# Kernel tuning notes

Hardware: AMD Instinct MI355X
Metric: run time of the kernel (lower is better)

The kernel has to match this reference:

```python
import jax, jax.numpy as jnp
import numpy as np

N, IN_C, E = 50000, 512, 800000
H, C = 2, 64          # heads, per-head channels
HC = H * C            # 128
OUT_C = 2
B = 64                # number of graphs
EPS = 1e-5
NEG_SLOPE = 0.2


def gat_conv(x, src, dst, W, a_src, a_dst, bias):
    """PyG GATConv (concat=True, add_self_loops already included in src/dst)."""
    n = x.shape[0]
    h = (x @ W).reshape(n, H, C)                      # [N,H,C]
    alpha_src = (h * a_src[None]).sum(-1)             # [N,H]
    alpha_dst = (h * a_dst[None]).sum(-1)             # [N,H]
    e = jax.nn.leaky_relu(alpha_src[src] + alpha_dst[dst], NEG_SLOPE)  # [E,H]
    # segment softmax over incoming edges of each destination node
    m = jax.ops.segment_max(e, dst, num_segments=n)   # [N,H]
    ex = jnp.exp(e - m[dst])
    denom = jax.ops.segment_sum(ex, dst, num_segments=n)
    alpha = ex / denom[dst]                           # [E,H]
    msg = h[src] * alpha[:, :, None]                  # [E,H,C]
    out = jax.ops.segment_sum(msg, dst, num_segments=n)  # [N,H,C]
    return out.reshape(n, HC) + bias


def batch_norm(x, gamma, beta):
    # BatchNorm1d in training mode: batch statistics over the node dim
    mu = x.mean(0)
    var = x.var(0)
    return gamma * (x - mu) * jax.lax.rsqrt(var + EPS) + beta


def setup_inputs() -> dict:
    key = jax.random.key(0)
    ks = jax.random.split(key, 16)
    x = jax.random.normal(ks[0], (N, IN_C), dtype=jnp.float32)
    edge_index = jax.random.randint(ks[1], (2, E), 0, N, dtype=jnp.int64)
    batch = jnp.sort(jax.random.randint(ks[2], (N,), 0, B, dtype=jnp.int64))
    g = lambda k, sh, fan: jax.random.normal(k, sh, dtype=jnp.float32) * (1.0 / np.sqrt(fan))
    return {
        "x": x, "edge_index": edge_index, "batch": batch,
        "W1": g(ks[3], (IN_C, HC), IN_C),
        "att_src1": g(ks[4], (H, C), C), "att_dst1": g(ks[5], (H, C), C),
        "b1": jnp.zeros((HC,), jnp.float32),
        "gamma1": jnp.ones((HC,), jnp.float32), "beta1": jnp.zeros((HC,), jnp.float32),
        "W2": g(ks[6], (HC, HC), HC),
        "att_src2": g(ks[7], (H, C), C), "att_dst2": g(ks[8], (H, C), C),
        "b2": jnp.zeros((HC,), jnp.float32),
        "gamma2": jnp.ones((HC,), jnp.float32), "beta2": jnp.zeros((HC,), jnp.float32),
        "Wlin": g(ks[9], (HC, OUT_C), HC),
        "blin": jnp.zeros((OUT_C,), jnp.float32),
    }


def reference(x, edge_index, batch, W1, att_src1, att_dst1, b1, gamma1, beta1,
              W2, att_src2, att_dst2, b2, gamma2, beta2, Wlin, blin):
    n = x.shape[0]
    # GATConv adds self-loops by default
    loop = jnp.arange(n, dtype=edge_index.dtype)
    src = jnp.concatenate([edge_index[0], loop])
    dst = jnp.concatenate([edge_index[1], loop])

    h = gat_conv(x, src, dst, W1, att_src1, att_dst1, b1)
    h = jax.nn.relu(batch_norm(h, gamma1, beta1))
    h = gat_conv(h, src, dst, W2, att_src2, att_dst2, b2)
    h = jax.nn.relu(batch_norm(h, gamma2, beta2))

    # global mean pool over graphs
    sums = jax.ops.segment_sum(h, batch, num_segments=B)           # [B,HC]
    cnt = jax.ops.segment_sum(jnp.ones((n,), h.dtype), batch, num_segments=B)
    pooled = sums / jnp.maximum(cnt, 1.0)[:, None]
    return pooled @ Wlin + blin                                    # [B,OUT_C]
```

## Files before the change

kernel.cpp:

```cpp
#include <hip/hip_runtime.h>
#include <hip/hip_bf16.h>
#include <cstdint>
#include <cstddef>

#define NN      50000
#define IN_C    512
#define EE      800000
#define ETOT    850000
#define HH      2
#define CC      64
#define HC      128
#define BB      64
#define OUTC    2
#define NEG_SLOPE 0.2f
#define BN_EPS  1e-5f

#define NBLK_SCAN ((NN + 255) / 256)

#define NXCD     8
#define NPX      ((NN + NXCD - 1) / NXCD)
#define EDGES_PER_SLOT 2048
#define NSLOT    ((ETOT + EDGES_PER_SLOT - 1) / EDGES_PER_SLOT)
#define WFRG_BLKS ((IN_C * 16 + HC * 16 + 255) / 256)

typedef __bf16 bf16x8 __attribute__((ext_vector_type(8)));
typedef float  f32x4  __attribute__((ext_vector_type(4)));

__device__ __forceinline__ unsigned f2bf(float f) {
    __bf16 b = (__bf16)f;
    return (unsigned)__builtin_bit_cast(unsigned short, b);
}

__device__ __forceinline__ void gload_lds16(const float* g, float* l) {
    __builtin_amdgcn_global_load_lds(
        (const __attribute__((address_space(1))) unsigned*)g,
        (__attribute__((address_space(3))) unsigned*)l,
        16, 0, 0);
}

__global__ __launch_bounds__(256) void prep_kernel(
    const float* __restrict__ W1, unsigned short* __restrict__ Wf1,
    const float* __restrict__ W2, unsigned short* __restrict__ Wf2,
    const int* __restrict__ ei, int* __restrict__ deg)
{
    if (blockIdx.x < WFRG_BLKS) {
        int t = blockIdx.x * 256 + threadIdx.x;
        const float* W; unsigned short* Wf;
        if (t < IN_C * 16) { W = W1; Wf = Wf1; }
        else {
            t -= IN_C * 16;
            if (t >= HC * 16) return;
            W = W2; Wf = Wf2;
        }
        int lane = t & 63, frag = t >> 6;
        int kblk = frag >> 3, nt = frag & 7;
        int quad = lane >> 4, ln = lane & 15;
        int kbase = kblk * 32 + quad * 8;
        int n = nt * 16 + ln;
        unsigned short u[8];
#pragma unroll
        for (int j = 0; j < 8; ++j)
            u[j] = (unsigned short)f2bf(W[(size_t)(kbase + j) * HC + n]);
        ushort4 a; a.x = u[0]; a.y = u[1]; a.z = u[2]; a.w = u[3];
        ushort4 b; b.x = u[4]; b.y = u[5]; b.z = u[6]; b.w = u[7];
        *(ushort4*)(Wf + (size_t)t * 8)     = a;
        *(ushort4*)(Wf + (size_t)t * 8 + 4) = b;
        return;
    }
    const int bid  = blockIdx.x - WFRG_BLKS;
    const int xcd  = bid & (NXCD - 1);
    const int slot = bid >> 3;
    const int lo = xcd * NPX, hi = lo + NPX;
    const int base = slot * EDGES_PER_SLOT;
#pragma unroll
    for (int it = 0; it < EDGES_PER_SLOT / 256; ++it) {
        int e = base + it * 256 + threadIdx.x;
        if (e < ETOT) {
            int d = (e < EE) ? ei[EE + e] : (e - EE);
            if (d >= lo && d < hi) atomicAdd(&deg[d], 1);
        }
    }
}

__global__ __launch_bounds__(256) void bsum_kernel(const int* __restrict__ deg, int* __restrict__ bsum)
{
    int i = blockIdx.x * 256 + threadIdx.x;
    int v = (i < NN) ? deg[i] : 0;
    int lane = threadIdx.x & 63, wv = threadIdx.x >> 6;
#pragma unroll
    for (int o = 32; o > 0; o >>= 1) v += __shfl_down(v, o);
    __shared__ int ws[4];
    if (lane == 0) ws[wv] = v;
    __syncthreads();
    if (threadIdx.x == 0) bsum[blockIdx.x] = ws[0] + ws[1] + ws[2] + ws[3];
}

__global__ __launch_bounds__(256) void bscan_kernel(
    const int* __restrict__ bsum, int* __restrict__ bofs, int* __restrict__ rowp)
{
    int t = threadIdx.x;
    int lane = t & 63, wv = t >> 6;
    int v = (t < NBLK_SCAN) ? bsum[t] : 0;
    int x = v;
#pragma unroll
    for (int o = 1; o < 64; o <<= 1) {
        int y = __shfl_up(x, o);
        if (lane >= o) x += y;
    }
    __shared__ int ws[4];
    if (lane == 63) ws[wv] = x;
    __syncthreads();
    int wo = 0;
#pragma unroll
    for (int w = 0; w < 4; ++w) if (w < wv) wo += ws[w];
    if (t < NBLK_SCAN) bofs[t] = x + wo - v;
    if (t == 0) rowp[NN] = ETOT;
}

__global__ __launch_bounds__(256) void bapply_kernel(
    const int* __restrict__ deg, const int* __restrict__ bofs,
    int* __restrict__ rowp, int* __restrict__ cur)
{
    int i = blockIdx.x * 256 + threadIdx.x;
    int v = (i < NN) ? deg[i] : 0;
    int lane = threadIdx.x & 63, wv = threadIdx.x >> 6;
    int x = v;
#pragma unroll
    for (int o = 1; o < 64; o <<= 1) {
        int y = __shfl_up(x, o);
        if (lane >= o) x += y;
    }
    __shared__ int ws[4];
    if (lane == 63) ws[wv] = x;
    __syncthreads();
    int wo = 0;
#pragma unroll
    for (int w = 0; w < 4; ++w) if (w < wv) wo += ws[w];
    if (i < NN) {
        int r = bofs[blockIdx.x] + x + wo - v;
        rowp[i] = r; cur[i] = r;
    }
}

__global__ __launch_bounds__(256) void scatter_kernel(
    const int* __restrict__ ei, int* __restrict__ cur, int* __restrict__ esrc)
{
    const int xcd  = blockIdx.x & (NXCD - 1);
    const int slot = blockIdx.x >> 3;
    const int lo = xcd * NPX, hi = lo + NPX;
    const int base = slot * EDGES_PER_SLOT;
#pragma unroll
    for (int it = 0; it < EDGES_PER_SLOT / 256; ++it) {
        int e = base + it * 256 + threadIdx.x;
        if (e < ETOT) {
            int s, d;
            if (e < EE) { s = ei[e]; d = ei[EE + e]; }
            else        { s = e - EE; d = s; }
            if (d >= lo && d < hi) {
                int pos = atomicAdd(&cur[d], 1);
                esrc[pos] = s;
            }
        }
    }
}

template<int K, bool AFFINE>
__global__ __launch_bounds__(256) void mfma_gemm_kernel(
    const float* __restrict__ A, const unsigned short* __restrict__ Wf,
    const float* __restrict__ atts, const float* __restrict__ attd,
    unsigned* __restrict__ hb, float* __restrict__ as_, float* __restrict__ ad_,
    const float* __restrict__ sc, const float* __restrict__ sh)
{
    constexpr int NSTEP = K >> 5;
    __shared__ __align__(16) float Abuf[2][64 * 64];

    const int tid  = threadIdx.x;
    const int wave = tid >> 6, lane = tid & 63;
    const int quad = lane >> 4, ln = lane & 15;
    const int m0 = blockIdx.x * 64;

    const int srow = tid >> 3;
    const int g    = (tid & 7) ^ (srow & 7);
    int grow0 = m0 + srow;      if (grow0 > NN - 1) grow0 = NN - 1;
    int grow1 = m0 + srow + 32; if (grow1 > NN - 1) grow1 = NN - 1;
    const float* gsrc0 = A + (size_t)grow0 * K + g * 4;
    const float* gsrc1 = A + (size_t)grow1 * K + g * 4;

    const int rr = wave * 16 + ln;
    const int base_f = rr * 32;
    const int sA = (((quad * 2)     ^ (rr & 7)) * 4);
    const int sB = (((quad * 2 + 1) ^ (rr & 7)) * 4);

    const unsigned short* wbase = Wf + lane * 8;

    f32x4 acc[8];
#pragma unroll
    for (int nt = 0; nt < 8; ++nt) acc[nt] = (f32x4){0.f, 0.f, 0.f, 0.f};

    gload_lds16(gsrc0,      &Abuf[0][wave * 256]);
    gload_lds16(gsrc1,      &Abuf[0][1024 + wave * 256]);
    gload_lds16(gsrc0 + 32, &Abuf[0][2048 + wave * 256]);
    gload_lds16(gsrc1 + 32, &Abuf[0][3072 + wave * 256]);
    bf16x8 bfr[2][8];
#pragma unroll
    for (int nt = 0; nt < 8; ++nt) bfr[0][nt] = *(const bf16x8*)(wbase + nt * 512);

#pragma unroll
    for (int ks = 0; ks < NSTEP; ++ks) {
        const int sub  = ks & 1;
        const int cbuf = (ks >> 1) & 1;
        const int bsel = ks & 1;
        if (sub == 0) {
            __syncthreads();
            if (ks + 2 < NSTEP) {
                const float* n0 = gsrc0 + (size_t)(ks + 2) * 32;
                const float* n1 = gsrc1 + (size_t)(ks + 2) * 32;
                float* db = &Abuf[cbuf ^ 1][wave * 256];
                gload_lds16(n0,      db);
                gload_lds16(n1,      db + 1024);
                gload_lds16(n0 + 32, db + 2048);
                gload_lds16(n1 + 32, db + 3072);
            }
        }

        const float* fb_base = &Abuf[cbuf][sub * 2048 + base_f];
        float4 fa = *(const float4*)(fb_base + sA);
        float4 fb = *(const float4*)(fb_base + sB);
        float va[8] = {fa.x, fa.y, fa.z, fa.w, fb.x, fb.y, fb.z, fb.w};
        if (AFFINE) {
            const int kk = ks * 32 + quad * 8;
            const float4 s0 = *(const float4*)(sc + kk), s1 = *(const float4*)(sc + kk + 4);
            const float4 h0 = *(const float4*)(sh + kk), h1 = *(const float4*)(sh + kk + 4);
            va[0] = fmaxf(fmaf(s0.x, va[0], h0.x), 0.f);
            va[1] = fmaxf(fmaf(s0.y, va[1], h0.y), 0.f);
            va[2] = fmaxf(fmaf(s0.z, va[2], h0.z), 0.f);
            va[3] = fmaxf(fmaf(s0.w, va[3], h0.w), 0.f);
            va[4] = fmaxf(fmaf(s1.x, va[4], h1.x), 0.f);
            va[5] = fmaxf(fmaf(s1.y, va[5], h1.y), 0.f);
            va[6] = fmaxf(fmaf(s1.z, va[6], h1.z), 0.f);
            va[7] = fmaxf(fmaf(s1.w, va[7], h1.w), 0.f);
        }
        union { bf16x8 v; unsigned short u[8]; } af;
#pragma unroll
        for (int j = 0; j < 8; ++j) af.u[j] = (unsigned short)f2bf(va[j]);

        if (ks + 1 < NSTEP) {
            const unsigned short* wfp = wbase + (size_t)(ks + 1) * 4096;
#pragma unroll
            for (int nt = 0; nt < 8; ++nt)
                bfr[bsel ^ 1][nt] = *(const bf16x8*)(wfp + nt * 512);
        }

#pragma unroll
        for (int nt = 0; nt < 8; ++nt)
            acc[nt] = __builtin_amdgcn_mfma_f32_16x16x32_bf16(af.v, bfr[bsel][nt], acc[nt], 0, 0, 0);
    }

    float wsv[8], wdv[8];
#pragma unroll
    for (int nt = 0; nt < 8; ++nt) { wsv[nt] = atts[nt * 16 + ln]; wdv[nt] = attd[nt * 16 + ln]; }

    const int mbase = m0 + wave * 16 + quad * 4;
#pragma unroll
    for (int r = 0; r < 4; ++r) {
        int m = mbase + r;
        bool ok = (m < NN);
        float ps0 = 0.f, ps1 = 0.f, pd0 = 0.f, pd1 = 0.f;
#pragma unroll
        for (int nt = 0; nt < 8; ++nt) {
            float v = acc[nt][r];
            if (nt < 4) { ps0 = fmaf(v, wsv[nt], ps0); pd0 = fmaf(v, wdv[nt], pd0); }
            else        { ps1 = fmaf(v, wsv[nt], ps1); pd1 = fmaf(v, wdv[nt], pd1); }
        }
#pragma unroll
        for (int nt = 0; nt < 4; ++nt) {
            unsigned pk = f2bf(acc[nt][r]) | (f2bf(acc[nt + 4][r]) << 16);
            if (ok) hb[(size_t)m * 64 + nt * 16 + ln] = pk;
        }
#pragma unroll
        for (int o = 8; o > 0; o >>= 1) {
            ps0 += __shfl_down(ps0, o); ps1 += __shfl_down(ps1, o);
            pd0 += __shfl_down(pd0, o); pd1 += __shfl_down(pd1, o);
        }
        if (ok && ln == 0) {
            *(float2*)&as_[m * 2] = make_float2(ps0, ps1);
            *(float2*)&ad_[m * 2] = make_float2(pd0, pd1);
        }
    }
}

__global__ __launch_bounds__(256) void gat_agg_kernel(
    const int* __restrict__ rowp, const int* __restrict__ esrc,
    const float* __restrict__ as_, const float* __restrict__ ad_,
    const unsigned* __restrict__ hb, float* __restrict__ out,
    float* __restrict__ stats)
{
    const int tid  = threadIdx.x;
    const int wave = tid >> 6;
    const int lane = tid & 63;
    const int half = lane >> 5;
    const int hl   = lane & 31;
    const int node = blockIdx.x * 8 + wave * 2 + half;

    const int beg = rowp[node], end = rowp[node + 1];
    float2 adv = *(const float2*)&ad_[node * 2];

    const int deg = end - beg;
    const int degmax = max(deg, __shfl_xor(deg, 32));
    const int nchunk = (degmax + 31) >> 5;
    const int sb = half * 32;
    const unsigned* hbp = hb + 2 * hl;

    float l0 = 0.f, l1 = 0.f;
    float a00 = 0.f, a01 = 0.f, a10 = 0.f, a11 = 0.f;

    for (int c = 0; c < nchunk; ++c) {
        int j0 = beg + c * 32;
        int sl = 0; float p0l = 0.f, p1l = 0.f;
        if (j0 + hl < end) {
            sl = esrc[j0 + hl];
            float2 t = *(const float2*)&as_[sl * 2];
            float e0 = t.x + adv.x; e0 = fmaxf(e0, NEG_SLOPE * e0);
            float e1 = t.y + adv.y; e1 = fmaxf(e1, NEG_SLOPE * e1);
            p0l = __expf(e0); p1l = __expf(e1);
        }
        l0 += p0l; l1 += p1l;

        int nj = end - j0; nj = nj < 0 ? 0 : (nj > 32 ? 32 : nj);
        int njmax = max(nj, __shfl_xor(nj, 32));

        int j = 0;
        for (; j + 16 <= njmax; j += 16) {
            uint2 u[16];
#pragma unroll
            for (int q = 0; q < 16; ++q) {
                int s = __shfl(sl, sb + j + q);
                u[q]  = *(const uint2*)(hbp + (size_t)s * 64);
            }
#pragma unroll
            for (int q = 0; q < 16; ++q) {
                float p0 = __shfl(p0l, sb + j + q);
                float p1 = __shfl(p1l, sb + j + q);
                a00 = fmaf(p0, __uint_as_float(u[q].x << 16), a00);
                a10 = fmaf(p1, __uint_as_float(u[q].x & 0xffff0000u), a10);
                a01 = fmaf(p0, __uint_as_float(u[q].y << 16), a01);
                a11 = fmaf(p1, __uint_as_float(u[q].y & 0xffff0000u), a11);
            }
        }
        for (; j + 4 <= njmax; j += 4) {
            uint2 u[4];
#pragma unroll
            for (int q = 0; q < 4; ++q) {
                int s = __shfl(sl, sb + j + q);
                u[q]  = *(const uint2*)(hbp + (size_t)s * 64);
            }
#pragma unroll
            for (int q = 0; q < 4; ++q) {
                float p0 = __shfl(p0l, sb + j + q);
                float p1 = __shfl(p1l, sb + j + q);
                a00 = fmaf(p0, __uint_as_float(u[q].x << 16), a00);
                a10 = fmaf(p1, __uint_as_float(u[q].x & 0xffff0000u), a10);
                a01 = fmaf(p0, __uint_as_float(u[q].y << 16), a01);
                a11 = fmaf(p1, __uint_as_float(u[q].y & 0xffff0000u), a11);
            }
        }
        for (; j < njmax; ++j) {
            int s  = __shfl(sl, sb + j);
            float p0 = __shfl(p0l, sb + j);
            float p1 = __shfl(p1l, sb + j);
            uint2 u = *(const uint2*)(hbp + (size_t)s * 64);
            a00 = fmaf(p0, __uint_as_float(u.x << 16), a00);
            a10 = fmaf(p1, __uint_as_float(u.x & 0xffff0000u), a10);
            a01 = fmaf(p0, __uint_as_float(u.y << 16), a01);
            a11 = fmaf(p1, __uint_as_float(u.y & 0xffff0000u), a11);
        }
    }

#pragma unroll
    for (int o = 1; o < 32; o <<= 1) {
        l0 += __shfl_xor(l0, o); l1 += __shfl_xor(l1, o);
    }
    float r0 = 1.f / l0, r1 = 1.f / l1;
    float v00 = a00 * r0, v01 = a01 * r0, v10 = a10 * r1, v11 = a11 * r1;
    *(float2*)&out[(size_t)node * HC + 2 * hl]      = make_float2(v00, v01);
    *(float2*)&out[(size_t)node * HC + 64 + 2 * hl] = make_float2(v10, v11);

    __shared__ float red[8][128];
    const int w2 = wave * 2 + half;
    red[w2][2 * hl]      = v00;  red[w2][2 * hl + 1]      = v01;
    red[w2][64 + 2 * hl] = v10;  red[w2][64 + 2 * hl + 1] = v11;
    __syncthreads();
    if (tid < 128) {
        float s = 0.f, q = 0.f;
#pragma unroll
        for (int w = 0; w < 8; ++w) {
            float v = red[w][tid];
            s += v; q = fmaf(v, v, q);
        }
        int slot = blockIdx.x & 63;
        atomicAdd(&stats[slot * 128 + tid], s);
        atomicAdd(&stats[64 * 128 + slot * 128 + tid], q);
    }
}

__global__ void bn_params_kernel(
    const float* __restrict__ stats, const float* __restrict__ gamma,
    const float* __restrict__ beta, float* __restrict__ sc, float* __restrict__ sh)
{
    int c = threadIdx.x;
    float su = 0.f, sq = 0.f;
#pragma unroll
    for (int k = 0; k < 64; ++k) {
        su += stats[k * 128 + c];
        sq += stats[64 * 128 + k * 128 + c];
    }
    const float inv_n = 1.0f / (float)NN;
    float mu = su * inv_n;
    float var = sq * inv_n - mu * mu;
    float rs = rsqrtf(var + BN_EPS);
    float s = gamma[c] * rs;
    sc[c] = s;
    sh[c] = beta[c] - mu * s;
}

__global__ __launch_bounds__(256) void pool_kernel(
    const float* __restrict__ x, const float* __restrict__ sc,
    const float* __restrict__ sh, const int* __restrict__ batch,
    float* __restrict__ pool, float* __restrict__ cnt)
{
    int c = threadIdx.x & 127;
    int half = threadIdx.x >> 7;
    int r0 = blockIdx.x * 64;
    int rend = min(r0 + 64, NN);
    float s = sc[c], b = sh[c];
    int cur = -1; float acc = 0.f, ccount = 0.f;
    for (int r = r0 + half; r < rend; r += 2) {
        int g = batch[r];
        if (g != cur) {
            if (cur >= 0) {
                atomicAdd(&pool[cur * HC + c], acc);
                if (c == 0) atomicAdd(&cnt[cur], ccount);
            }
            cur = g; acc = 0.f; ccount = 0.f;
        }
        float v = x[(size_t)r * HC + c];
        acc += fmaxf(fmaf(s, v, b), 0.f);
        ccount += 1.f;
    }
    if (cur >= 0) {
        atomicAdd(&pool[cur * HC + c], acc);
        if (c == 0) atomicAdd(&cnt[cur], ccount);
    }
}

__global__ void final_kernel(
    const float* __restrict__ pool, const float* __restrict__ cnt,
    const float* __restrict__ Wlin, const float* __restrict__ blin,
    float* __restrict__ outp)
{
    int t = threadIdx.x;
    int b = t >> 1, oc = t & 1;
    float inv = 1.f / fmaxf(cnt[b], 1.f);
    float s = blin[oc];
    for (int c = 0; c < HC; ++c)
        s += pool[b * HC + c] * inv * Wlin[c * 2 + oc];
    outp[b * 2 + oc] = s;
}

static constexpr size_t OFF_OUT   = 0;
static constexpr size_t OFF_AS    = OFF_OUT + (size_t)NN*HC;
static constexpr size_t OFF_AD    = OFF_AS  + (size_t)NN*HH;
static constexpr size_t OFF_ST1   = OFF_AD  + (size_t)NN*HH;
static constexpr size_t OFF_ST2   = OFF_ST1 + 2*64*128;
static constexpr size_t OFF_SC1   = OFF_ST2 + 2*64*128;
static constexpr size_t OFF_SH1   = OFF_SC1 + 128;
static constexpr size_t OFF_SC2   = OFF_SH1 + 128;
static constexpr size_t OFF_SH2   = OFF_SC2 + 128;
static constexpr size_t OFF_POOL  = OFF_SH2 + 128;
static constexpr size_t OFF_CNT   = OFF_POOL+ (size_t)BB*HC;
static constexpr size_t OFF_ZEND  = OFF_CNT + BB;
static constexpr size_t IOFF_DEG  = 0;
static constexpr size_t IOFF_ROWP = IOFF_DEG  + NN;
static constexpr size_t IOFF_CUR  = IOFF_ROWP + NN + 1;
static constexpr size_t IOFF_BSUM = IOFF_CUR  + NN;
static constexpr size_t IOFF_BOFS = IOFF_BSUM + NBLK_SCAN;
static constexpr size_t IOFF_ESRC = IOFF_BOFS + NBLK_SCAN;
static constexpr size_t IOFF_HB   = (IOFF_ESRC + ETOT + 3) & ~(size_t)3;
static constexpr size_t IOFF_WF1  = IOFF_HB + (size_t)NN*64;
static constexpr size_t IOFF_WF2  = IOFF_WF1 + (size_t)IN_C*64;
static constexpr size_t IOFF_END  = IOFF_WF2 + (size_t)HC*64;

extern "C" void kernel_launch(void* const* d_in, const int* in_sizes, int n_in,
                              void* d_out, int out_size, void* d_ws, size_t ws_size,
                              hipStream_t stream)
{
    const float* x       = (const float*)d_in[0];
    const int*   ei      = (const int*)  d_in[1];
    const int*   batch   = (const int*)  d_in[2];
    const float* W1      = (const float*)d_in[3];
    const float* atts1   = (const float*)d_in[4];
    const float* attd1   = (const float*)d_in[5];
    const float* gamma1  = (const float*)d_in[7];
    const float* beta1   = (const float*)d_in[8];
    const float* W2      = (const float*)d_in[9];
    const float* atts2   = (const float*)d_in[10];
    const float* attd2   = (const float*)d_in[11];
    const float* gamma2  = (const float*)d_in[13];
    const float* beta2   = (const float*)d_in[14];
    const float* Wlin    = (const float*)d_in[15];
    const float* blin    = (const float*)d_in[16];
    float* outp = (float*)d_out;

    float* ws    = (float*)d_ws;
    float* out   = ws + OFF_OUT;
    float* as_   = ws + OFF_AS;
    float* ad_   = ws + OFF_AD;
    float* st1   = ws + OFF_ST1;
    float* st2   = ws + OFF_ST2;
    float* sc1   = ws + OFF_SC1;
    float* sh1   = ws + OFF_SH1;
    float* sc2   = ws + OFF_SC2;
    float* sh2   = ws + OFF_SH2;
    float* pool  = ws + OFF_POOL;
    float* cnt   = ws + OFF_CNT;

    int* iws  = (int*)(ws + OFF_ZEND);
    int* deg  = iws + IOFF_DEG;
    int* rowp = iws + IOFF_ROWP;
    int* curp = iws + IOFF_CUR;
    int* bsum = iws + IOFF_BSUM;
    int* bofs = iws + IOFF_BOFS;
    int* esrc = iws + IOFF_ESRC;
    unsigned* hb = (unsigned*)(iws + IOFF_HB);
    unsigned short* Wf1 = (unsigned short*)(iws + IOFF_WF1);
    unsigned short* Wf2 = (unsigned short*)(iws + IOFF_WF2);

    const int BIN_BLK   = NXCD * NSLOT;
    const int GEMM_BLK  = (NN + 63) / 64;
    const int WAVE_BLK  = NN / 8;
    const int POOL_BLK  = (NN + 63) / 64;

    hipMemsetAsync(st1, 0, (OFF_ZEND - OFF_ST1) * sizeof(float) + NN * sizeof(int), stream);

    prep_kernel<<<WFRG_BLKS + BIN_BLK, 256, 0, stream>>>(W1, Wf1, W2, Wf2, ei, deg);
    bsum_kernel<<<NBLK_SCAN, 256, 0, stream>>>(deg, bsum);
    bscan_kernel<<<1, 256, 0, stream>>>(bsum, bofs, rowp);
    bapply_kernel<<<NBLK_SCAN, 256, 0, stream>>>(deg, bofs, rowp, curp);
    scatter_kernel<<<BIN_BLK, 256, 0, stream>>>(ei, curp, esrc);

    mfma_gemm_kernel<IN_C, false><<<GEMM_BLK, 256, 0, stream>>>(
        x, Wf1, atts1, attd1, hb, as_, ad_, nullptr, nullptr);
    gat_agg_kernel<<<WAVE_BLK, 256, 0, stream>>>(rowp, esrc, as_, ad_, hb, out, st1);
    bn_params_kernel<<<1, 128, 0, stream>>>(st1, gamma1, beta1, sc1, sh1);

    mfma_gemm_kernel<HC, true><<<GEMM_BLK, 256, 0, stream>>>(
        out, Wf2, atts2, attd2, hb, as_, ad_, sc1, sh1);
    gat_agg_kernel<<<WAVE_BLK, 256, 0, stream>>>(rowp, esrc, as_, ad_, hb, out, st2);
    bn_params_kernel<<<1, 128, 0, stream>>>(st2, gamma2, beta2, sc2, sh2);

    pool_kernel<<<POOL_BLK, 256, 0, stream>>>(out, sc2, sh2, batch, pool, cnt);
    final_kernel<<<1, 128, 0, stream>>>(pool, cnt, Wlin, blin, outp);
}
```

Before: 413.9 us.

## Fuse edge scatter into first GEMM launch and fold BN params into consumers

The CSR scatter blocks are prepended to the layer-1 GEMM grid so edge binning runs concurrently with the dense projection instead of as a separate launch. The standalone bn_params kernels are removed. Each GEMM2 block and each pool block now reduces the per-slot stats itself, computing scale and shift into LDS or registers. This cuts three launches and the serialization between them, at the cost of redundant per-block stats reduction and mixed workloads in one grid.

```diff
diff --git a/kernel.cpp b/kernel.cpp
--- a/kernel.cpp
+++ b/kernel.cpp
@@ -21,6 +21,7 @@
 #define NPX      ((NN + NXCD - 1) / NXCD)
 #define EDGES_PER_SLOT 2048
 #define NSLOT    ((ETOT + EDGES_PER_SLOT - 1) / EDGES_PER_SLOT)
+#define BIN_BLKS (NXCD * NSLOT)
 #define WFRG_BLKS ((IN_C * 16 + HC * 16 + 255) / 256)
 
 typedef __bf16 bf16x8 __attribute__((ext_vector_type(8)));
@@ -142,42 +143,62 @@
     }
 }
 
-__global__ __launch_bounds__(256) void scatter_kernel(
-    const int* __restrict__ ei, int* __restrict__ cur, int* __restrict__ esrc)
-{
-    const int xcd  = blockIdx.x & (NXCD - 1);
-    const int slot = blockIdx.x >> 3;
-    const int lo = xcd * NPX, hi = lo + NPX;
-    const int base = slot * EDGES_PER_SLOT;
-#pragma unroll
-    for (int it = 0; it < EDGES_PER_SLOT / 256; ++it) {
-        int e = base + it * 256 + threadIdx.x;
-        if (e < ETOT) {
-            int s, d;
-            if (e < EE) { s = ei[e]; d = ei[EE + e]; }
-            else        { s = e - EE; d = s; }
-            if (d >= lo && d < hi) {
-                int pos = atomicAdd(&cur[d], 1);
-                esrc[pos] = s;
-            }
-        }
-    }
-}
-
-template<int K, bool AFFINE>
+template<int K, bool AFFINE, bool SCATTER>
 __global__ __launch_bounds__(256) void mfma_gemm_kernel(
     const float* __restrict__ A, const unsigned short* __restrict__ Wf,
     const float* __restrict__ atts, const float* __restrict__ attd,
     unsigned* __restrict__ hb, float* __restrict__ as_, float* __restrict__ ad_,
-    const float* __restrict__ sc, const float* __restrict__ sh)
-{
+    const float* __restrict__ stats, const float* __restrict__ gamma,
+    const float* __restrict__ beta,
+    const int* __restrict__ ei, int* __restrict__ curp, int* __restrict__ esrc)
+{
+    if (SCATTER && blockIdx.x < BIN_BLKS) {
+        const int bid  = blockIdx.x;
+        const int xcd  = bid & (NXCD - 1);
+        const int slot = bid >> 3;
+        const int lo = xcd * NPX, hi = lo + NPX;
+        const int base = slot * EDGES_PER_SLOT;
+#pragma unroll
+        for (int it = 0; it < EDGES_PER_SLOT / 256; ++it) {
+            int e = base + it * 256 + threadIdx.x;
+            if (e < ETOT) {
+                int s, d;
+                if (e < EE) { s = ei[e]; d = ei[EE + e]; }
+                else        { s = e - EE; d = s; }
+                if (d >= lo && d < hi) {
+                    int pos = atomicAdd(&curp[d], 1);
+                    esrc[pos] = s;
+                }
+            }
+        }
+        return;
+    }
+    const int gblk = SCATTER ? ((int)blockIdx.x - BIN_BLKS) : (int)blockIdx.x;
+
     constexpr int NSTEP = K >> 5;
     __shared__ __align__(16) float Abuf[2][64 * 64];
+    __shared__ __align__(16) float scl[AFFINE ? HC : 4], shl[AFFINE ? HC : 4];
 
     const int tid  = threadIdx.x;
     const int wave = tid >> 6, lane = tid & 63;
     const int quad = lane >> 4, ln = lane & 15;
-    const int m0 = blockIdx.x * 64;
+    const int m0 = gblk * 64;
+
+    if (AFFINE && tid < HC) {
+        float su = 0.f, sq = 0.f;
+#pragma unroll
+        for (int k = 0; k < 64; ++k) {
+            su += stats[k * 128 + tid];
+            sq += stats[64 * 128 + k * 128 + tid];
+        }
+        const float inv_n = 1.0f / (float)NN;
+        float mu = su * inv_n;
+        float var = sq * inv_n - mu * mu;
+        float rs = rsqrtf(var + BN_EPS);
+        float s = gamma[tid] * rs;
+        scl[tid] = s;
+        shl[tid] = beta[tid] - mu * s;
+    }
 
     const int srow = tid >> 3;
     const int g    = (tid & 7) ^ (srow & 7);
@@ -229,8 +250,8 @@
         float va[8] = {fa.x, fa.y, fa.z, fa.w, fb.x, fb.y, fb.z, fb.w};
         if (AFFINE) {
             const int kk = ks * 32 + quad * 8;
-            const float4 s0 = *(const float4*)(sc + kk), s1 = *(const float4*)(sc + kk + 4);
-            const float4 h0 = *(const float4*)(sh + kk), h1 = *(const float4*)(sh + kk + 4);
+            const float4 s0 = *(const float4*)(&scl[kk]), s1 = *(const float4*)(&scl[kk + 4]);
+            const float4 h0 = *(const float4*)(&shl[kk]), h1 = *(const float4*)(&shl[kk + 4]);
             va[0] = fmaxf(fmaf(s0.x, va[0], h0.x), 0.f);
             va[1] = fmaxf(fmaf(s0.y, va[1], h0.y), 0.f);
             va[2] = fmaxf(fmaf(s0.z, va[2], h0.z), 0.f);
@@ -403,11 +424,15 @@
     }
 }
 
-__global__ void bn_params_kernel(
-    const float* __restrict__ stats, const float* __restrict__ gamma,
-    const float* __restrict__ beta, float* __restrict__ sc, float* __restrict__ sh)
-{
-    int c = threadIdx.x;
+__global__ __launch_bounds__(256) void pool_kernel(
+    const float* __restrict__ x, const float* __restrict__ stats,
+    const float* __restrict__ gamma, const float* __restrict__ beta,
+    const int* __restrict__ batch,
+    float* __restrict__ pool, float* __restrict__ cnt)
+{
+    int c = threadIdx.x & 127;
+    int half = threadIdx.x >> 7;
+
     float su = 0.f, sq = 0.f;
 #pragma unroll
     for (int k = 0; k < 64; ++k) {
@@ -419,20 +444,10 @@
     float var = sq * inv_n - mu * mu;
     float rs = rsqrtf(var + BN_EPS);
     float s = gamma[c] * rs;
-    sc[c] = s;
-    sh[c] = beta[c] - mu * s;
-}
-
-__global__ __launch_bounds__(256) void pool_kernel(
-    const float* __restrict__ x, const float* __restrict__ sc,
-    const float* __restrict__ sh, const int* __restrict__ batch,
-    float* __restrict__ pool, float* __restrict__ cnt)
-{
-    int c = threadIdx.x & 127;
-    int half = threadIdx.x >> 7;
+    float b = beta[c] - mu * s;
+
     int r0 = blockIdx.x * 64;
     int rend = min(r0 + 64, NN);
-    float s = sc[c], b = sh[c];
     int cur = -1; float acc = 0.f, ccount = 0.f;
     for (int r = r0 + half; r < rend; r += 2) {
         int g = batch[r];
@@ -472,11 +487,7 @@
 static constexpr size_t OFF_AD    = OFF_AS  + (size_t)NN*HH;
 static constexpr size_t OFF_ST1   = OFF_AD  + (size_t)NN*HH;
 static constexpr size_t OFF_ST2   = OFF_ST1 + 2*64*128;
-static constexpr size_t OFF_SC1   = OFF_ST2 + 2*64*128;
-static constexpr size_t OFF_SH1   = OFF_SC1 + 128;
-static constexpr size_t OFF_SC2   = OFF_SH1 + 128;
-static constexpr size_t OFF_SH2   = OFF_SC2 + 128;
-static constexpr size_t OFF_POOL  = OFF_SH2 + 128;
+static constexpr size_t OFF_POOL  = OFF_ST2 + 2*64*128;
 static constexpr size_t OFF_CNT   = OFF_POOL+ (size_t)BB*HC;
 static constexpr size_t OFF_ZEND  = OFF_CNT + BB;
 static constexpr size_t IOFF_DEG  = 0;
@@ -517,10 +528,6 @@
     float* ad_   = ws + OFF_AD;
     float* st1   = ws + OFF_ST1;
     float* st2   = ws + OFF_ST2;
-    float* sc1   = ws + OFF_SC1;
-    float* sh1   = ws + OFF_SH1;
-    float* sc2   = ws + OFF_SC2;
-    float* sh2   = ws + OFF_SH2;
     float* pool  = ws + OFF_POOL;
     float* cnt   = ws + OFF_CNT;
 
@@ -535,29 +542,27 @@
     unsigned short* Wf1 = (unsigned short*)(iws + IOFF_WF1);
     unsigned short* Wf2 = (unsigned short*)(iws + IOFF_WF2);
 
-    const int BIN_BLK   = NXCD * NSLOT;
     const int GEMM_BLK  = (NN + 63) / 64;
     const int WAVE_BLK  = NN / 8;
     const int POOL_BLK  = (NN + 63) / 64;
 
     hipMemsetAsync(st1, 0, (OFF_ZEND - OFF_ST1) * sizeof(float) + NN * sizeof(int), stream);
 
-    prep_kernel<<<WFRG_BLKS + BIN_BLK, 256, 0, stream>>>(W1, Wf1, W2, Wf2, ei, deg);
+    prep_kernel<<<WFRG_BLKS + BIN_BLKS, 256, 0, stream>>>(W1, Wf1, W2, Wf2, ei, deg);
     bsum_kernel<<<NBLK_SCAN, 256, 0, stream>>>(deg, bsum);
     bscan_kernel<<<1, 256, 0, stream>>>(bsum, bofs, rowp);
     bapply_kernel<<<NBLK_SCAN, 256, 0, stream>>>(deg, bofs, rowp, curp);
-    scatter_kernel<<<BIN_BLK, 256, 0, stream>>>(ei, curp, esrc);
-
-    mfma_gemm_kernel<IN_C, false><<<GEMM_BLK, 256, 0, stream>>>(
-        x, Wf1, atts1, attd1, hb, as_, ad_, nullptr, nullptr);
+
+    mfma_gemm_kernel<IN_C, false, true><<<BIN_BLKS + GEMM_BLK, 256, 0, stream>>>(
+        x, Wf1, atts1, attd1, hb, as_, ad_,
+        nullptr, nullptr, nullptr, ei, curp, esrc);
     gat_agg_kernel<<<WAVE_BLK, 256, 0, stream>>>(rowp, esrc, as_, ad_, hb, out, st1);
-    bn_params_kernel<<<1, 128, 0, stream>>>(st1, gamma1, beta1, sc1, sh1);
-
-    mfma_gemm_kernel<HC, true><<<GEMM_BLK, 256, 0, stream>>>(
-        out, Wf2, atts2, attd2, hb, as_, ad_, sc1, sh1);
+
+    mfma_gemm_kernel<HC, true, false><<<GEMM_BLK, 256, 0, stream>>>(
+        out, Wf2, atts2, attd2, hb, as_, ad_,
+        st1, gamma1, beta1, nullptr, nullptr, nullptr);
     gat_agg_kernel<<<WAVE_BLK, 256, 0, stream>>>(rowp, esrc, as_, ad_, hb, out, st2);
-    bn_params_kernel<<<1, 128, 0, stream>>>(st2, gamma2, beta2, sc2, sh2);
-
-    pool_kernel<<<POOL_BLK, 256, 0, stream>>>(out, sc2, sh2, batch, pool, cnt);
+
+    pool_kernel<<<POOL_BLK, 256, 0, stream>>>(out, st2, gamma2, beta2, batch, pool, cnt);
     final_kernel<<<1, 128, 0, stream>>>(pool, cnt, Wlin, blin, outp);
 }
```

New measurement: 416.5 us. Within noise of the previous version (+0.6%).
